# Optimization experiments

Measured on AMD Instinct MI355X. Metric: run time of the kernel, lower is better.

The kernel has to match this reference:

```python
import jax, jax.numpy as jnp
import numpy as np

N_NODES = 20000
N_EDGES = 160000
MUL0, MUL1 = 32, 16          # 32x0e + 16x1o for both in and out irreps
EDGE_FEAT = 128
HIDDEN = 128
W_SIZES = [MUL0*MUL0, MUL1*MUL0, MUL0*MUL1, MUL1*MUL1, MUL1*MUL1]  # uvw weights per path (sh muls are 1)
W_OFF = np.cumsum([0] + W_SIZES).tolist()
W_NUMEL = W_OFF[-1]          # 2560
EPS_LN = 1e-5

_e = np.zeros((3, 3, 3), np.float32)
for i, j, k in [(0, 1, 2), (1, 2, 0), (2, 0, 1)]:
    _e[i, j, k] = 1.0
    _e[i, k, j] = -1.0
EPS3 = jnp.asarray(_e)  # Levi-Civita for 1o x 1o -> 1o path


def setup_inputs() -> dict:
    key = jax.random.key(0)
    ks = jax.random.split(key, 8)
    node_attr = jax.random.normal(ks[0], (N_NODES, MUL0 + 3 * MUL1), jnp.float32)
    edge_index = jax.random.randint(ks[1], (2, N_EDGES), 0, N_NODES)
    edge_attr = jax.random.normal(ks[2], (N_EDGES, EDGE_FEAT), jnp.float32)
    edge_sh = jax.random.normal(ks[3], (N_EDGES, 4), jnp.float32)
    s1 = float(1.0 / np.sqrt(EDGE_FEAT))
    s2 = float(1.0 / np.sqrt(HIDDEN))
    fc_w1 = jax.random.uniform(ks[4], (EDGE_FEAT, HIDDEN), jnp.float32, -s1, s1)
    fc_b1 = jnp.zeros((HIDDEN,), jnp.float32)
    fc_w2 = jax.random.uniform(ks[5], (HIDDEN, W_NUMEL), jnp.float32, -s2, s2)
    fc_b2 = jnp.zeros((W_NUMEL,), jnp.float32)
    # LayerNorm params: mean_shift is ones for scalar (0e) irreps, zeros for 1o
    mean_shift = jnp.concatenate(
        [jnp.ones((1, MUL0, 1), jnp.float32), jnp.zeros((1, MUL1, 1), jnp.float32)], axis=1)
    affine_weight = jnp.ones((MUL0 + MUL1,), jnp.float32) + 0.1 * jax.random.normal(ks[6], (MUL0 + MUL1,), jnp.float32)
    affine_bias = 0.02 * jax.random.normal(ks[7], (MUL0,), jnp.float32)
    return dict(node_attr=node_attr, edge_attr=edge_attr, edge_sh=edge_sh,
                fc_w1=fc_w1, fc_b1=fc_b1, fc_w2=fc_w2, fc_b2=fc_b2,
                mean_shift=mean_shift, affine_weight=affine_weight,
                affine_bias=affine_bias, edge_index=edge_index)


def _forward(node_attr, edge_attr, edge_sh, fc_w1, fc_b1, fc_w2, fc_b2,
             mean_shift, affine_weight, affine_bias, edge_index):
    edge_src, edge_dst = edge_index[0], edge_index[1]
    # gather source-of-message node features per edge
    x = node_attr[edge_dst]                          # [E, 80]
    x0 = x[:, :MUL0]                                 # [E, 32]   l=0 scalars
    x1 = x[:, MUL0:].reshape(-1, MUL1, 3)            # [E, 16, 3] l=1 vectors
    sh0 = edge_sh[:, 0]                              # [E]
    sh1 = edge_sh[:, 1:4]                            # [E, 3]

    # per-edge TP weights from edge features (SimpleLinear: Lin-ReLU-Lin, dropout=0)
    w = jnp.maximum(edge_attr @ fc_w1 + fc_b1, 0.0) @ fc_w2 + fc_b2   # [E, 2560]
    w1 = w[:, W_OFF[0]:W_OFF[1]].reshape(-1, MUL0, MUL0)
    w2 = w[:, W_OFF[1]:W_OFF[2]].reshape(-1, MUL1, MUL0)
    w3 = w[:, W_OFF[2]:W_OFF[3]].reshape(-1, MUL0, MUL1)
    w4 = w[:, W_OFF[3]:W_OFF[4]].reshape(-1, MUL1, MUL1)
    w5 = w[:, W_OFF[4]:W_OFF[5]].reshape(-1, MUL1, MUL1)

    # e3nn FullyConnectedTensorProduct normalization (component + element):
    # coeff = sqrt(ir_out.dim / sum_of_fan_in_over_paths_to_that_output)
    c0 = float(np.sqrt(1.0 / (MUL0 + MUL1)))            # -> 0e: fan 32+16
    c1 = float(np.sqrt(3.0 / (MUL0 + MUL1 + MUL1)))     # -> 1o: fan 32+16+16
    is3 = float(1.0 / np.sqrt(3.0))  # wigner-3j (110),(011),(101)
    is6 = float(1.0 / np.sqrt(6.0))  # wigner-3j (111)

    out0 = c0 * (jnp.einsum('eu,e,euw->ew', x0, sh0, w1)
                 + is3 * jnp.einsum('eui,ei,euw->ew', x1, sh1, w2))            # [E, 32]
    out1 = c1 * (is3 * jnp.einsum('eu,ek,euw->ewk', x0, sh1, w3)
                 + is3 * jnp.einsum('eui,e,euw->ewi', x1, sh0, w4)
                 + is6 * jnp.einsum('ijk,eui,ej,euw->ewk', EPS3, x1, sh1, w5)) # [E, 16, 3]
    tp = jnp.concatenate([out0, out1.reshape(-1, MUL1 * 3)], axis=-1)          # [E, 80]

    # scatter-mean over destination (edge_src) nodes
    seg = jax.ops.segment_sum(tp, edge_src, num_segments=N_NODES)
    cnt = jax.ops.segment_sum(jnp.ones((tp.shape[0],), tp.dtype), edge_src, num_segments=N_NODES)
    out = seg / jnp.maximum(cnt, 1.0)[:, None]

    # residual (out irreps == in irreps, so F.pad is a no-op)
    out = out + node_attr

    # equivariant LayerNorm (normalization='component')
    f0 = out[:, :MUL0].reshape(-1, MUL0, 1)
    f0 = f0 - jnp.mean(f0, axis=1, keepdims=True) * mean_shift[:, :MUL0]
    n0 = jnp.mean(jnp.mean(f0 * f0, axis=-1), axis=1, keepdims=True)           # [N, 1]
    n0 = jax.lax.rsqrt(n0 + EPS_LN) * affine_weight[None, :MUL0]               # [N, 32]
    f0 = f0 * n0[:, :, None] + affine_bias[None, :, None]

    f1 = out[:, MUL0:].reshape(-1, MUL1, 3)
    f1 = f1 - jnp.mean(f1, axis=1, keepdims=True) * mean_shift[:, MUL0:]       # mean_shift=0 here
    n1 = jnp.mean(jnp.mean(f1 * f1, axis=-1), axis=1, keepdims=True)
    n1 = jax.lax.rsqrt(n1 + EPS_LN) * affine_weight[None, MUL0:]
    f1 = f1 * n1[:, :, None]

    return jnp.concatenate([f0.reshape(-1, MUL0), f1.reshape(-1, MUL1 * 3)], axis=-1)


def reference(node_attr, edge_attr, edge_sh, fc_w1, fc_b1, fc_w2, fc_b2,
              mean_shift, affine_weight, affine_bias, edge_index):
    return _forward(node_attr, edge_attr, edge_sh, fc_w1, fc_b1, fc_w2, fc_b2,
                    mean_shift, affine_weight, affine_bias, edge_index)
```

## Files before the change

### kernel.cpp

```cpp
#include <hip/hip_runtime.h>

typedef __attribute__((ext_vector_type(8))) short short8;
typedef __attribute__((ext_vector_type(4))) short bfx4;
typedef __attribute__((ext_vector_type(4))) float floatx4;

#define N_NODES 20000
#define N_EDGES 160000
#define TILE_E 64
#define EBLK (N_EDGES / TILE_E)

#define C0f   0.14433756729740643f
#define C1f   0.21650635094610965f
#define IS3   0.5773502691896258f
#define IS6   0.4082482904638631f
#define EPS_LN 1e-5f

#define W1F_OFF 0
#define W2F_OFF 32768
#define CNT_OFF 688128

__device__ __forceinline__ short f2bf(float f) {
    unsigned u = __float_as_uint(f);
    u += 0x7fff + ((u >> 16) & 1);
    return (short)(u >> 16);
}
__device__ __forceinline__ float bf2f(short s) {
    return __uint_as_float(((unsigned)(unsigned short)s) << 16);
}

__device__ __forceinline__ short8 load8_bf16(const float* p) {
    const float4* q = (const float4*)p;
    float4 f0 = q[0], f1 = q[1];
    short8 s;
    s[0]=f2bf(f0.x); s[1]=f2bf(f0.y); s[2]=f2bf(f0.z); s[3]=f2bf(f0.w);
    s[4]=f2bf(f1.x); s[5]=f2bf(f1.y); s[6]=f2bf(f1.z); s[7]=f2bf(f1.w);
    return s;
}

__device__ __forceinline__ floatx4 mfma4(const short8* a, short8 b0, short8 b1,
                                         short8 b2, short8 b3, float bias) {
    floatx4 C = {bias, bias, bias, bias};
    C = __builtin_amdgcn_mfma_f32_16x16x32_bf16(a[0], b0, C, 0, 0, 0);
    C = __builtin_amdgcn_mfma_f32_16x16x32_bf16(a[1], b1, C, 0, 0, 0);
    C = __builtin_amdgcn_mfma_f32_16x16x32_bf16(a[2], b2, C, 0, 0, 0);
    C = __builtin_amdgcn_mfma_f32_16x16x32_bf16(a[3], b3, C, 0, 0, 0);
    return C;
}

__global__ __launch_bounds__(256)
void prep_kernel(const float* __restrict__ fc_w1, const float* __restrict__ fc_w2,
                 short* __restrict__ w1f, short* __restrict__ w2f,
                 float* __restrict__ cnt) {
    int g = blockIdx.x * 256 + threadIdx.x;
    if (g < N_NODES) cnt[g] = 0.0f;
    if (g < 2048) {
        int ln = g & 15, qd = (g >> 4) & 3, kt = (g >> 6) & 3, t = g >> 8;
        int n = t * 16 + ln, kb = kt * 32 + qd * 8;
        short8 s;
        #pragma unroll
        for (int j = 0; j < 8; ++j) s[j] = f2bf(fc_w1[(kb + j) * 128 + n]);
        *(short8*)(w1f + g * 8) = s;
        return;
    }
    int g2 = g - 2048;
    if (g2 < 40960) {
        int ln = g2 & 15, qd = (g2 >> 4) & 3, kt = (g2 >> 6) & 3, t = g2 >> 8;
        int n = t * 16 + ln, kb = kt * 32 + qd * 8;
        short8 s;
        #pragma unroll
        for (int j = 0; j < 8; ++j) s[j] = f2bf(fc_w2[(kb + j) * 2560 + n]);
        *(short8*)(w2f + g2 * 8) = s;
    }
}

__global__ __launch_bounds__(128, 2)
void edge_kernel(const float* __restrict__ node_attr,
                 const float* __restrict__ edge_attr,
                 const float* __restrict__ edge_sh,
                 const float* __restrict__ fc_b1,
                 const float* __restrict__ fc_b2,
                 const int*   __restrict__ edge_index,
                 const short* __restrict__ w1f,
                 const short* __restrict__ w2f,
                 float* __restrict__ accum,
                 float* __restrict__ cnt)
{
    __shared__ short s_H[64 * 136];
    __shared__ short s_x0t[32 * 64];
    __shared__ short s_x1t[48 * 64];
    __shared__ short s_x1dt[16 * 64];
    __shared__ float s_sh[64 * 4];
    __shared__ int   s_src[64];
    __shared__ int   s_dst[64];

    const int tid = threadIdx.x;
    const int e0  = blockIdx.x * TILE_E;

    if (tid < 64) {
        int s = edge_index[e0 + tid];
        int d = edge_index[N_EDGES + e0 + tid];
        s_src[tid] = s; s_dst[tid] = d;
        atomicAdd(&cnt[s], 1.0f);
    }
    s_sh[tid]       = edge_sh[(size_t)e0 * 4 + tid];
    s_sh[tid + 128] = edge_sh[(size_t)e0 * 4 + tid + 128];
    __syncthreads();

    #pragma unroll
    for (int i = 0; i < 40; ++i) {
        int f = tid + i * 128;
        int e = f / 80, c = f % 80;
        float v = node_attr[(size_t)s_dst[e] * 80 + c];
        if (c < 32) s_x0t[c * 64 + e] = f2bf(v);
        else        s_x1t[(c - 32) * 64 + e] = f2bf(v);
    }
    #pragma unroll
    for (int i = 0; i < 8; ++i) {
        int it = tid + i * 128;
        int e = it >> 4, u = it & 15;
        const float* xp = node_attr + (size_t)s_dst[e] * 80 + 32 + u * 3;
        float d = xp[0] * s_sh[e*4+1] + xp[1] * s_sh[e*4+2] + xp[2] * s_sh[e*4+3];
        s_x1dt[u * 64 + e] = f2bf(d);
    }
    __syncthreads();

    const int lane = tid & 63;
    const int wv   = tid >> 6;
    const int ln   = lane & 15;
    const int qd   = lane >> 4;
    const int eb0  = wv * 32 + qd * 4;
    const int eb1  = eb0 + 16;

    {
        short8 a1[2][4];
        #pragma unroll
        for (int g = 0; g < 2; ++g) {
            const float* ap = edge_attr + (size_t)(e0 + wv*32 + g*16 + ln) * 128 + qd * 8;
            #pragma unroll
            for (int kt = 0; kt < 4; ++kt) a1[g][kt] = load8_bf16(ap + kt * 32);
        }
        #pragma unroll
        for (int t = 0; t < 8; ++t) {
            const short* bp = w1f + t * 2048 + lane * 8;
            short8 b0 = *(const short8*)bp;
            short8 b1 = *(const short8*)(bp + 512);
            short8 b2 = *(const short8*)(bp + 1024);
            short8 b3 = *(const short8*)(bp + 1536);
            float bias = fc_b1[t * 16 + ln];
            #pragma unroll
            for (int g = 0; g < 2; ++g) {
                floatx4 C = mfma4(a1[g], b0, b1, b2, b3, bias);
                #pragma unroll
                for (int r = 0; r < 4; ++r)
                    s_H[(wv*32 + g*16 + qd*4 + r) * 136 + t*16 + ln] = f2bf(fmaxf(C[r], 0.f));
            }
        }
    }
    __syncthreads();

    short8 a2[2][4];
    #pragma unroll
    for (int g = 0; g < 2; ++g) {
        const short* hp = s_H + (wv*32 + g*16 + ln) * 136 + qd * 8;
        #pragma unroll
        for (int kt = 0; kt < 4; ++kt) a2[g][kt] = *(const short8*)(hp + kt * 32);
    }

    const short* wbase = w2f + lane * 8;

    float r0lo[2][4] = {}, r0hi[2][4] = {}, r1lo[2][4] = {}, r1hi[2][4] = {};

    #pragma unroll 2
    for (int u = 0; u < 32; ++u) {
        const short* bp = wbase + (size_t)(2*u) * 2048;
        short8 L0 = *(const short8*)bp,          L1 = *(const short8*)(bp + 512);
        short8 L2 = *(const short8*)(bp + 1024), L3 = *(const short8*)(bp + 1536);
        short8 H0 = *(const short8*)(bp + 2048), H1 = *(const short8*)(bp + 2560);
        short8 H2 = *(const short8*)(bp + 3072), H3 = *(const short8*)(bp + 3584);
        float blo = fc_b2[2*u*16 + ln], bhi = fc_b2[2*u*16 + 16 + ln];
        #pragma unroll
        for (int g = 0; g < 2; ++g) {
            floatx4 Clo = mfma4(a2[g], L0, L1, L2, L3, blo);
            floatx4 Chi = mfma4(a2[g], H0, H1, H2, H3, bhi);
            bfx4 xs = *(const bfx4*)(s_x0t + u*64 + (g ? eb1 : eb0));
            #pragma unroll
            for (int r = 0; r < 4; ++r) {
                float a = bf2f(xs[r]);
                r0lo[g][r] += a * Clo[r];
                r0hi[g][r] += a * Chi[r];
            }
        }
    }
    #pragma unroll 2
    for (int u = 0; u < 16; ++u) {
        const short* bp = wbase + (size_t)(64 + 2*u) * 2048;
        short8 L0 = *(const short8*)bp,          L1 = *(const short8*)(bp + 512);
        short8 L2 = *(const short8*)(bp + 1024), L3 = *(const short8*)(bp + 1536);
        short8 H0 = *(const short8*)(bp + 2048), H1 = *(const short8*)(bp + 2560);
        short8 H2 = *(const short8*)(bp + 3072), H3 = *(const short8*)(bp + 3584);
        float blo = fc_b2[(64 + 2*u)*16 + ln], bhi = fc_b2[(64 + 2*u)*16 + 16 + ln];
        #pragma unroll
        for (int g = 0; g < 2; ++g) {
            floatx4 Clo = mfma4(a2[g], L0, L1, L2, L3, blo);
            floatx4 Chi = mfma4(a2[g], H0, H1, H2, H3, bhi);
            bfx4 xs = *(const bfx4*)(s_x1dt + u*64 + (g ? eb1 : eb0));
            #pragma unroll
            for (int r = 0; r < 4; ++r) {
                float a = bf2f(xs[r]);
                r1lo[g][r] += a * Clo[r];
                r1hi[g][r] += a * Chi[r];
            }
        }
    }
    #pragma unroll
    for (int g = 0; g < 2; ++g)
        #pragma unroll
        for (int r = 0; r < 4; ++r) {
            int e = (g ? eb1 : eb0) + r;
            float sh0 = s_sh[e*4];
            int base = s_src[e] * 80;
            atomicAdd(&accum[base + ln],      C0f * (sh0 * r0lo[g][r] + IS3 * r1lo[g][r]));
            atomicAdd(&accum[base + 16 + ln], C0f * (sh0 * r0hi[g][r] + IS3 * r1hi[g][r]));
        }

    float r3[2][4] = {};
    float r4[2][4][3] = {};
    float r5[2][4][3] = {};

    #pragma unroll 2
    for (int u = 0; u < 32; ++u) {
        const short* bp = wbase + (size_t)(96 + u) * 2048;
        short8 b0 = *(const short8*)bp,          b1 = *(const short8*)(bp + 512);
        short8 b2 = *(const short8*)(bp + 1024), b3 = *(const short8*)(bp + 1536);
        float bias = fc_b2[(96 + u)*16 + ln];
        #pragma unroll
        for (int g = 0; g < 2; ++g) {
            floatx4 C = mfma4(a2[g], b0, b1, b2, b3, bias);
            bfx4 xs = *(const bfx4*)(s_x0t + u*64 + (g ? eb1 : eb0));
            #pragma unroll
            for (int r = 0; r < 4; ++r)
                r3[g][r] += bf2f(xs[r]) * C[r];
        }
    }
    for (int u = 0; u < 16; ++u) {
        const short* bp4 = wbase + (size_t)(128 + u) * 2048;
        short8 F0 = *(const short8*)bp4,          F1 = *(const short8*)(bp4 + 512);
        short8 F2 = *(const short8*)(bp4 + 1024), F3 = *(const short8*)(bp4 + 1536);
        const short* bp5 = wbase + (size_t)(144 + u) * 2048;
        short8 G0 = *(const short8*)bp5,          G1 = *(const short8*)(bp5 + 512);
        short8 G2 = *(const short8*)(bp5 + 1024), G3 = *(const short8*)(bp5 + 1536);
        float b4 = fc_b2[(128 + u)*16 + ln], b5 = fc_b2[(144 + u)*16 + ln];
        #pragma unroll
        for (int g = 0; g < 2; ++g) {
            floatx4 C4 = mfma4(a2[g], F0, F1, F2, F3, b4);
            floatx4 C5 = mfma4(a2[g], G0, G1, G2, G3, b5);
            int eb = (g ? eb1 : eb0);
            bfx4 x0s = *(const bfx4*)(s_x1t + (u*3 + 0)*64 + eb);
            bfx4 x1s = *(const bfx4*)(s_x1t + (u*3 + 1)*64 + eb);
            bfx4 x2s = *(const bfx4*)(s_x1t + (u*3 + 2)*64 + eb);
            #pragma unroll
            for (int r = 0; r < 4; ++r) {
                float a0 = bf2f(x0s[r]), a1 = bf2f(x1s[r]), a2v = bf2f(x2s[r]);
                r4[g][r][0] += a0 * C4[r];  r5[g][r][0] += a0 * C5[r];
                r4[g][r][1] += a1 * C4[r];  r5[g][r][1] += a1 * C5[r];
                r4[g][r][2] += a2v * C4[r]; r5[g][r][2] += a2v * C5[r];
            }
        }
    }
    #pragma unroll
    for (int g = 0; g < 2; ++g)
        #pragma unroll
        for (int r = 0; r < 4; ++r) {
            int e = (g ? eb1 : eb0) + r;
            float sh0 = s_sh[e*4], sa = s_sh[e*4+1], sb = s_sh[e*4+2], sc = s_sh[e*4+3];
            int base = s_src[e] * 80;
            float t3 = C1f * IS3 * r3[g][r];
            float s0 = C1f * IS3 * sh0;
            float c6 = C1f * IS6;
            float v50 = r5[g][r][1] * sc - r5[g][r][2] * sb;
            float v51 = r5[g][r][2] * sa - r5[g][r][0] * sc;
            float v52 = r5[g][r][0] * sb - r5[g][r][1] * sa;
            atomicAdd(&accum[base + 32 + ln*3 + 0], sa * t3 + s0 * r4[g][r][0] + c6 * v50);
            atomicAdd(&accum[base + 32 + ln*3 + 1], sb * t3 + s0 * r4[g][r][1] + c6 * v51);
            atomicAdd(&accum[base + 32 + ln*3 + 2], sc * t3 + s0 * r4[g][r][2] + c6 * v52);
        }
}

__global__ __launch_bounds__(256)
void node_kernel(const float* __restrict__ node_attr,
                 const float* __restrict__ mean_shift,
                 const float* __restrict__ aw,
                 const float* __restrict__ ab,
                 const float* __restrict__ cnt,
                 float* __restrict__ out)
{
    int n = blockIdx.x * blockDim.x + threadIdx.x;
    if (n >= N_NODES) return;
    float inv = 1.0f / fmaxf(cnt[n], 1.0f);
    size_t base = (size_t)n * 80;
    float v[80];
    const float4* o4 = (const float4*)(out + base);
    const float4* a4 = (const float4*)(node_attr + base);
    #pragma unroll
    for (int i = 0; i < 20; ++i) {
        float4 o = o4[i], a = a4[i];
        v[4*i+0] = o.x * inv + a.x;
        v[4*i+1] = o.y * inv + a.y;
        v[4*i+2] = o.z * inv + a.z;
        v[4*i+3] = o.w * inv + a.w;
    }

    float m0 = 0.f;
    #pragma unroll
    for (int u = 0; u < 32; ++u) m0 += v[u];
    m0 *= (1.0f / 32.0f);
    float n0 = 0.f;
    #pragma unroll
    for (int u = 0; u < 32; ++u) {
        float f = v[u] - m0 * mean_shift[u];
        v[u] = f;
        n0 += f * f;
    }
    n0 = rsqrtf(n0 * (1.0f / 32.0f) + EPS_LN);
    #pragma unroll
    for (int u = 0; u < 32; ++u) v[u] = v[u] * (n0 * aw[u]) + ab[u];

    float m1[3] = {0.f, 0.f, 0.f};
    #pragma unroll
    for (int u = 0; u < 16; ++u)
        #pragma unroll
        for (int i = 0; i < 3; ++i) m1[i] += v[32 + u*3 + i];
    #pragma unroll
    for (int i = 0; i < 3; ++i) m1[i] *= (1.0f / 16.0f);
    float n1 = 0.f;
    #pragma unroll
    for (int u = 0; u < 16; ++u)
        #pragma unroll
        for (int i = 0; i < 3; ++i) {
            float f = v[32 + u*3 + i] - m1[i] * mean_shift[32 + u];
            v[32 + u*3 + i] = f;
            n1 += f * f;
        }
    n1 = rsqrtf(n1 * (1.0f / 48.0f) + EPS_LN);
    #pragma unroll
    for (int u = 0; u < 16; ++u)
        #pragma unroll
        for (int i = 0; i < 3; ++i)
            v[32 + u*3 + i] *= (n1 * aw[32 + u]);

    float4* w4 = (float4*)(out + base);
    #pragma unroll
    for (int i = 0; i < 20; ++i) {
        float4 o; o.x = v[4*i]; o.y = v[4*i+1]; o.z = v[4*i+2]; o.w = v[4*i+3];
        w4[i] = o;
    }
}

extern "C" void kernel_launch(void* const* d_in, const int* in_sizes, int n_in,
                              void* d_out, int out_size, void* d_ws, size_t ws_size,
                              hipStream_t stream) {
    const float* node_attr  = (const float*)d_in[0];
    const float* edge_attr  = (const float*)d_in[1];
    const float* edge_sh    = (const float*)d_in[2];
    const float* fc_w1      = (const float*)d_in[3];
    const float* fc_b1      = (const float*)d_in[4];
    const float* fc_w2      = (const float*)d_in[5];
    const float* fc_b2      = (const float*)d_in[6];
    const float* mean_shift = (const float*)d_in[7];
    const float* aw         = (const float*)d_in[8];
    const float* ab         = (const float*)d_in[9];
    const int*   edge_index = (const int*)d_in[10];
    float* out = (float*)d_out;

    short* w1f = (short*)((char*)d_ws + W1F_OFF);
    short* w2f = (short*)((char*)d_ws + W2F_OFF);
    float* cnt = (float*)((char*)d_ws + CNT_OFF);

    (void)hipMemsetAsync(d_out, 0, (size_t)N_NODES * 80 * sizeof(float), stream);

    prep_kernel<<<(2048 + 40960 + 255) / 256, 256, 0, stream>>>(fc_w1, fc_w2, w1f, w2f, cnt);
    edge_kernel<<<EBLK, 128, 0, stream>>>(node_attr, edge_attr, edge_sh,
                                          fc_b1, fc_b2, edge_index,
                                          w1f, w2f, out, cnt);
    node_kernel<<<(N_NODES + 255) / 256, 256, 0, stream>>>(node_attr, mean_shift,
                                                           aw, ab, cnt, out);
}
```

Measured before the change: 363.2 us.

## Alias shared buffers, swizzle node-feature tiles, raise occupancy to four blocks

Makes s_H and the transposed node-feature tiles share one LDS pool, gathering node features only after the hidden activations are loaded into registers. This shrinks per-block LDS, and launch bounds now request four blocks per CU instead of two. The transposed tiles also get an XOR swizzle on write and read to cut LDS bank conflicts on the scattered transposed stores. The tighter launch bound may force register spills, and the node gather now sits after the first GEMM rather than overlapping with it.

```diff
diff --git a/kernel.cpp b/kernel.cpp
--- a/kernel.cpp
+++ b/kernel.cpp
@@ -45,6 +45,13 @@
     C = __builtin_amdgcn_mfma_f32_16x16x32_bf16(a[2], b2, C, 0, 0, 0);
     C = __builtin_amdgcn_mfma_f32_16x16x32_bf16(a[3], b3, C, 0, 0, 0);
     return C;
+}
+
+__device__ __forceinline__ int xsw(int row, int e) {
+    return row * 64 + ((e & 3) | ((((e >> 2) ^ row) & 15) << 2));
+}
+__device__ __forceinline__ bfx4 ldx(const short* base, int row, int gran) {
+    return *(const bfx4*)(base + row * 64 + (((gran ^ row) & 15) << 2));
 }
 
 __global__ __launch_bounds__(256)
@@ -73,7 +80,7 @@
     }
 }
 
-__global__ __launch_bounds__(128, 2)
+__global__ __launch_bounds__(128, 4)
 void edge_kernel(const float* __restrict__ node_attr,
                  const float* __restrict__ edge_attr,
                  const float* __restrict__ edge_sh,
@@ -85,13 +92,15 @@
                  float* __restrict__ accum,
                  float* __restrict__ cnt)
 {
-    __shared__ short s_H[64 * 136];
-    __shared__ short s_x0t[32 * 64];
-    __shared__ short s_x1t[48 * 64];
-    __shared__ short s_x1dt[16 * 64];
+    __shared__ __align__(16) short s_pool[64 * 136];
     __shared__ float s_sh[64 * 4];
     __shared__ int   s_src[64];
     __shared__ int   s_dst[64];
+
+    short* s_H    = s_pool;
+    short* s_x0t  = s_pool;
+    short* s_x1t  = s_pool + 2048;
+    short* s_x1dt = s_pool + 5120;
 
     const int tid = threadIdx.x;
     const int e0  = blockIdx.x * TILE_E;
@@ -104,24 +113,6 @@
     }
     s_sh[tid]       = edge_sh[(size_t)e0 * 4 + tid];
     s_sh[tid + 128] = edge_sh[(size_t)e0 * 4 + tid + 128];
-    __syncthreads();
-
-    #pragma unroll
-    for (int i = 0; i < 40; ++i) {
-        int f = tid + i * 128;
-        int e = f / 80, c = f % 80;
-        float v = node_attr[(size_t)s_dst[e] * 80 + c];
-        if (c < 32) s_x0t[c * 64 + e] = f2bf(v);
-        else        s_x1t[(c - 32) * 64 + e] = f2bf(v);
-    }
-    #pragma unroll
-    for (int i = 0; i < 8; ++i) {
-        int it = tid + i * 128;
-        int e = it >> 4, u = it & 15;
-        const float* xp = node_attr + (size_t)s_dst[e] * 80 + 32 + u * 3;
-        float d = xp[0] * s_sh[e*4+1] + xp[1] * s_sh[e*4+2] + xp[2] * s_sh[e*4+3];
-        s_x1dt[u * 64 + e] = f2bf(d);
-    }
     __syncthreads();
 
     const int lane = tid & 63;
@@ -130,6 +121,8 @@
     const int qd   = lane >> 4;
     const int eb0  = wv * 32 + qd * 4;
     const int eb1  = eb0 + 16;
+    const int gr0  = eb0 >> 2;
+    const int gr1  = eb1 >> 2;
 
     {
         short8 a1[2][4];
@@ -156,7 +149,6 @@
             }
         }
     }
-    __syncthreads();
 
     short8 a2[2][4];
     #pragma unroll
@@ -165,6 +157,25 @@
         #pragma unroll
         for (int kt = 0; kt < 4; ++kt) a2[g][kt] = *(const short8*)(hp + kt * 32);
     }
+    __syncthreads();
+
+    #pragma unroll
+    for (int i = 0; i < 40; ++i) {
+        int f = tid + i * 128;
+        int e = f / 80, c = f % 80;
+        float v = node_attr[(size_t)s_dst[e] * 80 + c];
+        if (c < 32) s_x0t[xsw(c, e)] = f2bf(v);
+        else        s_x1t[xsw(c - 32, e)] = f2bf(v);
+    }
+    #pragma unroll
+    for (int i = 0; i < 8; ++i) {
+        int it = tid + i * 128;
+        int e = it >> 4, u = it & 15;
+        const float* xp = node_attr + (size_t)s_dst[e] * 80 + 32 + u * 3;
+        float d = xp[0] * s_sh[e*4+1] + xp[1] * s_sh[e*4+2] + xp[2] * s_sh[e*4+3];
+        s_x1dt[xsw(u, e)] = f2bf(d);
+    }
+    __syncthreads();
 
     const short* wbase = w2f + lane * 8;
 
@@ -182,7 +193,7 @@
         for (int g = 0; g < 2; ++g) {
             floatx4 Clo = mfma4(a2[g], L0, L1, L2, L3, blo);
             floatx4 Chi = mfma4(a2[g], H0, H1, H2, H3, bhi);
-            bfx4 xs = *(const bfx4*)(s_x0t + u*64 + (g ? eb1 : eb0));
+            bfx4 xs = ldx(s_x0t, u, g ? gr1 : gr0);
             #pragma unroll
             for (int r = 0; r < 4; ++r) {
                 float a = bf2f(xs[r]);
@@ -203,7 +214,7 @@
         for (int g = 0; g < 2; ++g) {
             floatx4 Clo = mfma4(a2[g], L0, L1, L2, L3, blo);
             floatx4 Chi = mfma4(a2[g], H0, H1, H2, H3, bhi);
-            bfx4 xs = *(const bfx4*)(s_x1dt + u*64 + (g ? eb1 : eb0));
+            bfx4 xs = ldx(s_x1dt, u, g ? gr1 : gr0);
             #pragma unroll
             for (int r = 0; r < 4; ++r) {
                 float a = bf2f(xs[r]);
@@ -236,7 +247,7 @@
         #pragma unroll
         for (int g = 0; g < 2; ++g) {
             floatx4 C = mfma4(a2[g], b0, b1, b2, b3, bias);
-            bfx4 xs = *(const bfx4*)(s_x0t + u*64 + (g ? eb1 : eb0));
+            bfx4 xs = ldx(s_x0t, u, g ? gr1 : gr0);
             #pragma unroll
             for (int r = 0; r < 4; ++r)
                 r3[g][r] += bf2f(xs[r]) * C[r];
@@ -254,10 +265,10 @@
         for (int g = 0; g < 2; ++g) {
             floatx4 C4 = mfma4(a2[g], F0, F1, F2, F3, b4);
             floatx4 C5 = mfma4(a2[g], G0, G1, G2, G3, b5);
-            int eb = (g ? eb1 : eb0);
-            bfx4 x0s = *(const bfx4*)(s_x1t + (u*3 + 0)*64 + eb);
-            bfx4 x1s = *(const bfx4*)(s_x1t + (u*3 + 1)*64 + eb);
-            bfx4 x2s = *(const bfx4*)(s_x1t + (u*3 + 2)*64 + eb);
+            int gr = (g ? gr1 : gr0);
+            bfx4 x0s = ldx(s_x1t, u*3 + 0, gr);
+            bfx4 x1s = ldx(s_x1t, u*3 + 1, gr);
+            bfx4 x2s = ldx(s_x1t, u*3 + 2, gr);
             #pragma unroll
             for (int r = 0; r < 4; ++r) {
                 float a0 = bf2f(x0s[r]), a1 = bf2f(x1s[r]), a2v = bf2f(x2s[r]);
```

Result: slower. 404.5 us (+11.4%).
